# Kernel tuning notes

Measured on AMD Instinct MI355X. Metric: run time of the kernel, lower is better.

The kernel has to match this reference:

```python
import jax, jax.numpy as jnp
import numpy as np

B, T, D, H = 512, 2048, 256, 256  # batch, seq_len, input_size, hidden_size


def _uniform(key, shape, fan_in):
    b = 1.0 / np.sqrt(fan_in)
    return jax.random.uniform(key, shape, minval=-b, maxval=b, dtype=jnp.float32)


def setup_inputs() -> dict:
    key = jax.random.key(0)
    ks = jax.random.split(key, 12)
    return {
        "input_tensor": jax.random.normal(ks[0], (B, T, D), dtype=jnp.float32),
        # fc_i: Linear(D, D)
        "Wi": _uniform(ks[1], (D, D), D), "bi": _uniform(ks[2], (D,), D),
        # fc_h: Linear(H, H)
        "Wh": _uniform(ks[3], (H, H), H), "bh": _uniform(ks[4], (H,), H),
        # fc_a: Linear(D, D)
        "Wa": _uniform(ks[5], (D, D), D), "ba": _uniform(ks[6], (D,), D),
        # LSTM(input_size=D, hidden_size=H), gates ordered [i, f, g, o]
        "W_ih": _uniform(ks[7], (4 * H, D), H), "b_ih": _uniform(ks[8], (4 * H,), H),
        "W_hh": _uniform(ks[9], (4 * H, H), H), "b_hh": _uniform(ks[10], (4 * H,), H),
    }


def reference(input_tensor, Wi, bi, Wh, bh, Wa, ba, W_ih, W_hh, b_ih, b_hh):
    x = input_tensor                      # (B, T, D)
    Bb = x.shape[0]
    Hh = Wh.shape[0]
    h0 = jnp.zeros((Bb, Hh), x.dtype)
    c0 = jnp.zeros((Bb, Hh), x.dtype)

    # Per-timestep FC attention; hidden state never updates in the loop,
    # so it vectorizes exactly over T.
    input_o = jnp.einsum('btd,ed->bte', x, Wi) + bi          # (B, T, D)
    hidden_o = h0 @ Wh.T + bh                                # (B, H) == (B, D)
    pre = input_o + hidden_o[:, None, :]                     # (B, T, D)
    attn = jax.nn.sigmoid(jnp.einsum('btd,ed->bte', pre, Wa) + ba)
    attention_output = jnp.sum(attn * x, axis=1)             # (B, D)

    # LSTM over a length-1 sequence (single cell step), PyTorch gate order i,f,g,o
    gates = attention_output @ W_ih.T + b_ih + h0 @ W_hh.T + b_hh
    i, f, g, o = jnp.split(gates, 4, axis=-1)
    i = jax.nn.sigmoid(i); f = jax.nn.sigmoid(f)
    g = jnp.tanh(g); o = jax.nn.sigmoid(o)
    c = f * c0 + i * g
    h = o * jnp.tanh(c)

    lstm_output = h[None]                                    # (1, B, H)
    return (lstm_output, h[None], c[None])
```

## Files before the change

### kernel.cpp

```cpp
#include <hip/hip_runtime.h>
#include <hip/hip_bf16.h>

typedef _Float16 f16x8 __attribute__((ext_vector_type(8)));
typedef float    f32x4 __attribute__((ext_vector_type(4)));

#define B_SZ 512
#define T_SZ 2048
#define D_SZ 256
#define TCHUNK 32
#define NCHUNK (T_SZ / TCHUNK)

__global__ __launch_bounds__(256) void prep_kernel(
    const float* __restrict__ Wa, const float* __restrict__ Wi,
    const float* __restrict__ bi, const float* __restrict__ bh,
    const float* __restrict__ ba,
    _Float16* __restrict__ Weff, float* __restrict__ beff)
{
    int e = blockIdx.x;
    int d = threadIdx.x;
    float a0 = 0.f, a1 = 0.f, a2 = 0.f, a3 = 0.f;
    #pragma unroll 4
    for (int k = 0; k < 256; k += 4) {
        a0 = fmaf(Wa[e*256 + k    ], Wi[(k    )*256 + d], a0);
        a1 = fmaf(Wa[e*256 + k + 1], Wi[(k + 1)*256 + d], a1);
        a2 = fmaf(Wa[e*256 + k + 2], Wi[(k + 2)*256 + d], a2);
        a3 = fmaf(Wa[e*256 + k + 3], Wi[(k + 3)*256 + d], a3);
    }
    Weff[e*256 + d] = (_Float16)((a0 + a1) + (a2 + a3));

    __shared__ float red[4];
    float s = Wa[e*256 + d] * (bi[d] + bh[d]);
    s += __shfl_down(s, 32, 64);
    s += __shfl_down(s, 16, 64);
    s += __shfl_down(s,  8, 64);
    s += __shfl_down(s,  4, 64);
    s += __shfl_down(s,  2, 64);
    s += __shfl_down(s,  1, 64);
    if ((d & 63) == 0) red[d >> 6] = s;
    __syncthreads();
    if (d == 0) beff[e] = ba[e] + ((red[0] + red[1]) + (red[2] + red[3]));
}

__global__ __launch_bounds__(1024, 4) void attn_kernel(
    const float* __restrict__ x,
    const _Float16* __restrict__ Weff,
    const float* __restrict__ beff,
    float* __restrict__ ao)
{
    const int b    = blockIdx.x;
    const int tid  = threadIdx.x;
    const int wave = tid >> 6;
    const int lane = tid & 63;
    const int l15  = lane & 15;
    const int lq   = lane >> 4;

    __shared__ _Float16 xs[TCHUNK * 256];
    char* xsb = reinterpret_cast<char*>(xs);

    const int col = wave*16 + l15;
    f16x8 bfrag[8];
    #pragma unroll
    for (int ks = 0; ks < 8; ++ks)
        bfrag[ks] = *reinterpret_cast<const f16x8*>(&Weff[col*256 + ks*32 + lq*8]);
    const float bcol = beff[col];

    const float* xb = x + (size_t)b * T_SZ * D_SZ;

    const int srow = tid >> 5;
    const int scg  = tid & 31;
    const float* srcp = xb + (size_t)srow * 256 + scg * 8;
    const int swb = (srow*512 + scg*16) ^ ((srow & 7) << 4);

    #define LOADC(R, c)                                                            \
        {                                                                          \
            const float* p = srcp + (size_t)(c) * (TCHUNK * D_SZ);                 \
            R##0 = *reinterpret_cast<const f32x4*>(p);                             \
            R##1 = *reinterpret_cast<const f32x4*>(p + 4);                         \
        }

    #define WRITE(R)                                                               \
        {                                                                          \
            f16x8 h;                                                               \
            h[0] = (_Float16)R##0[0]; h[1] = (_Float16)R##0[1];                    \
            h[2] = (_Float16)R##0[2]; h[3] = (_Float16)R##0[3];                    \
            h[4] = (_Float16)R##1[0]; h[5] = (_Float16)R##1[1];                    \
            h[6] = (_Float16)R##1[2]; h[7] = (_Float16)R##1[3];                    \
            *reinterpret_cast<f16x8*>(xsb + swb) = h;                              \
        }

    #define SYNC()                                                                 \
        {                                                                          \
            asm volatile("s_waitcnt lgkmcnt(0)" ::: "memory");                     \
            __builtin_amdgcn_sched_barrier(0);                                     \
            __builtin_amdgcn_s_barrier();                                          \
        }

    #define COMPUTE()                                                              \
        {                                                                          \
            _Pragma("unroll")                                                      \
            for (int rt = 0; rt < 2; ++rt) {                                       \
                const int arow  = rt*16 + l15;                                     \
                const int aswz  = (arow & 7) << 4;                                 \
                const int abase = arow * 512;                                      \
                f32x4 acc = {0.f, 0.f, 0.f, 0.f};                                  \
                _Pragma("unroll")                                                  \
                for (int ks = 0; ks < 8; ++ks) {                                   \
                    int ab = abase + ((ks*64 + lq*16) ^ aswz);                     \
                    f16x8 a = *reinterpret_cast<const f16x8*>(xsb + ab);           \
                    acc = __builtin_amdgcn_mfma_f32_16x16x32_f16(                  \
                        a, bfrag[ks], acc, 0, 0, 0);                               \
                }                                                                  \
                _Pragma("unroll")                                                  \
                for (int r = 0; r < 4; ++r) {                                      \
                    int row = rt*16 + lq*4 + r;                                    \
                    float s = acc[r] + bcol;                                       \
                    float attn = __builtin_amdgcn_rcpf(1.f + __expf(-s));          \
                    int cb = (row*512 + col*2) ^ ((row & 7) << 4);                 \
                    float xv = (float)*reinterpret_cast<const _Float16*>(xsb + cb);\
                    ao_acc = fmaf(attn, xv, ao_acc);                               \
                }                                                                  \
            }                                                                      \
        }

    float ao_acc = 0.f;
    f32x4 sA0, sA1, sB0, sB1;

    LOADC(sA, 0);
    LOADC(sB, 1);

    for (int c = 0; c < NCHUNK; c += 2) {
        WRITE(sA);
        SYNC();
        if (c + 2 < NCHUNK) LOADC(sA, c + 2);
        COMPUTE();
        SYNC();
        WRITE(sB);
        SYNC();
        if (c + 3 < NCHUNK) LOADC(sB, c + 3);
        COMPUTE();
        SYNC();
    }

    ao_acc += __shfl_xor(ao_acc, 16, 64);
    ao_acc += __shfl_xor(ao_acc, 32, 64);
    if (lq == 0) ao[b*256 + col] = ao_acc;

    #undef LOADC
    #undef WRITE
    #undef SYNC
    #undef COMPUTE
}

__global__ __launch_bounds__(256) void lstm_kernel(
    const float* __restrict__ ao,
    const float* __restrict__ Wih,
    const float* __restrict__ bih,
    const float* __restrict__ bhh,
    float* __restrict__ out)
{
    int b = blockIdx.x;
    int j = threadIdx.x;
    __shared__ float a[256];
    a[j] = ao[b*256 + j];
    __syncthreads();

    float gi = bih[j]       + bhh[j];
    float gg = bih[512 + j] + bhh[512 + j];
    float go = bih[768 + j] + bhh[768 + j];
    const float* wi = Wih + (size_t)j * 256;
    const float* wg = Wih + (size_t)(512 + j) * 256;
    const float* wo = Wih + (size_t)(768 + j) * 256;
    #pragma unroll 4
    for (int k = 0; k < 256; k += 4) {
        f32x4 w1 = *reinterpret_cast<const f32x4*>(wi + k);
        f32x4 w2 = *reinterpret_cast<const f32x4*>(wg + k);
        f32x4 w3 = *reinterpret_cast<const f32x4*>(wo + k);
        #pragma unroll
        for (int q = 0; q < 4; ++q) {
            float av = a[k + q];
            gi = fmaf(w1[q], av, gi);
            gg = fmaf(w2[q], av, gg);
            go = fmaf(w3[q], av, go);
        }
    }
    float ig = 1.f / (1.f + __expf(-gi));
    float g  = tanhf(gg);
    float og = 1.f / (1.f + __expf(-go));
    float cc = ig * g;
    float hh = og * tanhf(cc);
    out[          b*256 + j] = hh;
    out[131072 +  b*256 + j] = hh;
    out[262144 +  b*256 + j] = cc;
}

extern "C" void kernel_launch(void* const* d_in, const int* in_sizes, int n_in,
                              void* d_out, int out_size, void* d_ws, size_t ws_size,
                              hipStream_t stream) {
    const float* x    = (const float*)d_in[0];
    const float* Wi   = (const float*)d_in[1];
    const float* bi   = (const float*)d_in[2];
    const float* bh   = (const float*)d_in[4];
    const float* Wa   = (const float*)d_in[5];
    const float* ba   = (const float*)d_in[6];
    const float* W_ih = (const float*)d_in[7];
    const float* b_ih = (const float*)d_in[8];
    const float* b_hh = (const float*)d_in[10];

    char* ws = (char*)d_ws;
    _Float16* Weff = (_Float16*)ws;
    float*    beff = (float*)(ws + 128*1024);
    float*    ao   = (float*)(ws + 132*1024);

    prep_kernel<<<256, 256, 0, stream>>>(Wa, Wi, bi, bh, ba, Weff, beff);
    attn_kernel<<<B_SZ, 1024, 0, stream>>>(x, Weff, beff, ao);
    lstm_kernel<<<B_SZ, 256, 0, stream>>>(ao, W_ih, b_ih, b_hh, (float*)d_out);
}
```

Before: 295.0 us.

## Halve attn block size with each wave computing two column tiles per A fragment

The attention kernel moves from 1024 to 512 threads per block, and each wave now owns 32 output columns using two sets of B fragments. Each A fragment read from LDS feeds two MFMAs, which halves LDS reads per MFMA. The time chunk shrinks to 16 rows so the staging still maps one row per 32 threads. This doubles the weight registers per thread and halves rows per chunk, so there are more barrier rounds per block.

```diff
diff --git a/kernel.cpp b/kernel.cpp
--- a/kernel.cpp
+++ b/kernel.cpp
@@ -7,7 +7,7 @@
 #define B_SZ 512
 #define T_SZ 2048
 #define D_SZ 256
-#define TCHUNK 32
+#define TCHUNK 16
 #define NCHUNK (T_SZ / TCHUNK)
 
 __global__ __launch_bounds__(256) void prep_kernel(
@@ -41,7 +41,7 @@
     if (d == 0) beff[e] = ba[e] + ((red[0] + red[1]) + (red[2] + red[3]));
 }
 
-__global__ __launch_bounds__(1024, 4) void attn_kernel(
+__global__ __launch_bounds__(512, 4) void attn_kernel(
     const float* __restrict__ x,
     const _Float16* __restrict__ Weff,
     const float* __restrict__ beff,
@@ -57,12 +57,16 @@
     __shared__ _Float16 xs[TCHUNK * 256];
     char* xsb = reinterpret_cast<char*>(xs);
 
-    const int col = wave*16 + l15;
-    f16x8 bfrag[8];
+    const int col0 = wave*32 + l15;
+    const int col1 = col0 + 16;
+    f16x8 bfA[8], bfB[8];
     #pragma unroll
-    for (int ks = 0; ks < 8; ++ks)
-        bfrag[ks] = *reinterpret_cast<const f16x8*>(&Weff[col*256 + ks*32 + lq*8]);
-    const float bcol = beff[col];
+    for (int ks = 0; ks < 8; ++ks) {
+        bfA[ks] = *reinterpret_cast<const f16x8*>(&Weff[col0*256 + ks*32 + lq*8]);
+        bfB[ks] = *reinterpret_cast<const f16x8*>(&Weff[col1*256 + ks*32 + lq*8]);
+    }
+    const float bc0 = beff[col0];
+    const float bc1 = beff[col1];
 
     const float* xb = x + (size_t)b * T_SZ * D_SZ;
 
@@ -97,32 +101,41 @@
 
     #define COMPUTE()                                                              \
         {                                                                          \
+            const int arow  = l15;                                                 \
+            const int aswz  = (arow & 7) << 4;                                     \
+            const int abase = arow * 512;                                          \
+            f32x4 acc0 = {0.f, 0.f, 0.f, 0.f};                                     \
+            f32x4 acc1 = {0.f, 0.f, 0.f, 0.f};                                     \
             _Pragma("unroll")                                                      \
-            for (int rt = 0; rt < 2; ++rt) {                                       \
-                const int arow  = rt*16 + l15;                                     \
-                const int aswz  = (arow & 7) << 4;                                 \
-                const int abase = arow * 512;                                      \
-                f32x4 acc = {0.f, 0.f, 0.f, 0.f};                                  \
-                _Pragma("unroll")                                                  \
-                for (int ks = 0; ks < 8; ++ks) {                                   \
-                    int ab = abase + ((ks*64 + lq*16) ^ aswz);                     \
-                    f16x8 a = *reinterpret_cast<const f16x8*>(xsb + ab);           \
-                    acc = __builtin_amdgcn_mfma_f32_16x16x32_f16(                  \
-                        a, bfrag[ks], acc, 0, 0, 0);                               \
+            for (int ks = 0; ks < 8; ++ks) {                                       \
+                int ab = abase + ((ks*64 + lq*16) ^ aswz);                         \
+                f16x8 a = *reinterpret_cast<const f16x8*>(xsb + ab);               \
+                acc0 = __builtin_amdgcn_mfma_f32_16x16x32_f16(a, bfA[ks], acc0, 0, 0, 0); \
+                acc1 = __builtin_amdgcn_mfma_f32_16x16x32_f16(a, bfB[ks], acc1, 0, 0, 0); \
+            }                                                                      \
+            _Pragma("unroll")                                                      \
+            for (int r = 0; r < 4; ++r) {                                          \
+                int row  = lq*4 + r;                                               \
+                int rswz = (row & 7) << 4;                                         \
+                int rb   = row * 512;                                              \
+                {                                                                  \
+                    float s = acc0[r] + bc0;                                       \
+                    float attn = __builtin_amdgcn_rcpf(1.f + __expf(-s));          \
+                    float xv = (float)*reinterpret_cast<const _Float16*>(          \
+                        xsb + rb + ((col0*2) ^ rswz));                             \
+                    ao0 = fmaf(attn, xv, ao0);                                     \
                 }                                                                  \
-                _Pragma("unroll")                                                  \
-                for (int r = 0; r < 4; ++r) {                                      \
-                    int row = rt*16 + lq*4 + r;                                    \
-                    float s = acc[r] + bcol;                                       \
+                {                                                                  \
+                    float s = acc1[r] + bc1;                                       \
                     float attn = __builtin_amdgcn_rcpf(1.f + __expf(-s));          \
-                    int cb = (row*512 + col*2) ^ ((row & 7) << 4);                 \
-                    float xv = (float)*reinterpret_cast<const _Float16*>(xsb + cb);\
-                    ao_acc = fmaf(attn, xv, ao_acc);                               \
+                    float xv = (float)*reinterpret_cast<const _Float16*>(          \
+                        xsb + rb + ((col1*2) ^ rswz));                             \
+                    ao1 = fmaf(attn, xv, ao1);                                     \
                 }                                                                  \
             }                                                                      \
         }
 
-    float ao_acc = 0.f;
+    float ao0 = 0.f, ao1 = 0.f;
     f32x4 sA0, sA1, sB0, sB1;
 
     LOADC(sA, 0);
@@ -141,9 +154,14 @@
         SYNC();
     }
 
-    ao_acc += __shfl_xor(ao_acc, 16, 64);
-    ao_acc += __shfl_xor(ao_acc, 32, 64);
-    if (lq == 0) ao[b*256 + col] = ao_acc;
+    ao0 += __shfl_xor(ao0, 16, 64);
+    ao0 += __shfl_xor(ao0, 32, 64);
+    ao1 += __shfl_xor(ao1, 16, 64);
+    ao1 += __shfl_xor(ao1, 32, 64);
+    if (lq == 0) {
+        ao[b*256 + col0] = ao0;
+        ao[b*256 + col1] = ao1;
+    }
 
     #undef LOADC
     #undef WRITE
@@ -212,6 +230,6 @@
     float*    ao   = (float*)(ws + 132*1024);
 
     prep_kernel<<<256, 256, 0, stream>>>(Wa, Wi, bi, bh, ba, Weff, beff);
-    attn_kernel<<<B_SZ, 1024, 0, stream>>>(x, Weff, beff, ao);
+    attn_kernel<<<B_SZ, 512, 0, stream>>>(x, Weff, beff, ao);
     lstm_kernel<<<B_SZ, 256, 0, stream>>>(ao, W_ih, b_ih, b_hh, (float*)d_out);
 }
```

Result: faster. 264.8 us (-10.2%).
